# Kernel optimization log

Hardware: AMD Instinct MI355X
Metric: run time of the kernel (lower is better)

## Reference

```python
import jax, jax.numpy as jnp
import numpy as np

B, N = 2, 2000
C_IN, RH, RW = 256, 7, 7
D_FLAT = C_IN * RH * RW  # 12544
D_OUT = 1024
NUM_CLASSES = 10


def setup_inputs() -> dict:
    key = jax.random.key(0)
    ks = jax.random.split(key, 10)
    s1 = 1.0 / np.sqrt(D_FLAT)
    s2 = 1.0 / np.sqrt(D_OUT)
    return {
        "features": jax.random.normal(ks[0], (B, N, C_IN, RH, RW), jnp.float32),
        "boxes": jax.random.normal(ks[1], (B, N, 5), jnp.float32),
        "w1": jax.random.uniform(ks[2], (D_FLAT, D_OUT), jnp.float32, -s1, s1),
        "b1": jax.random.uniform(ks[3], (D_OUT,), jnp.float32, -s1, s1),
        "w2": jax.random.uniform(ks[4], (D_OUT, D_OUT), jnp.float32, -s2, s2),
        "b2": jax.random.uniform(ks[5], (D_OUT,), jnp.float32, -s2, s2),
        "wc": jax.random.uniform(ks[6], (D_OUT, NUM_CLASSES + 1), jnp.float32, -s2, s2),
        "bc": jax.random.uniform(ks[7], (NUM_CLASSES + 1,), jnp.float32, -s2, s2),
        "wr": jax.random.uniform(ks[8], (D_OUT, 5), jnp.float32, -s2, s2),
        "br": jax.random.uniform(ks[9], (5,), jnp.float32, -s2, s2),
    }


def reference(features, boxes, w1, b1, w2, b2, wc, bc, wr, br):
    # Flatten(start_dim=2): [B, N, C*7*7]
    x = features.reshape(B, N, D_FLAT)
    # fc: Linear -> ReLU -> Linear -> ReLU
    h = jax.nn.relu(jnp.einsum("bnd,de->bne", x, w1) + b1)
    h = jax.nn.relu(jnp.einsum("bnd,de->bne", h, w2) + b2)
    classification = jnp.einsum("bnd,dc->bnc", h, wc) + bc  # [B, N, num_classes+1]
    regression = jnp.einsum("bnd,dr->bnr", h, wr) + br      # [B, N, 5]
    boxes_out = boxes + regression
    rois = boxes
    return classification, boxes_out, rois
```

## Files before the change

### kernel.cpp

```cpp
#include <hip/hip_runtime.h>
#include <stdint.h>

#define GAS __attribute__((address_space(1)))
#define LAS __attribute__((address_space(3)))

typedef short bf16x8 __attribute__((ext_vector_type(8)));
typedef float f32x4 __attribute__((ext_vector_type(4)));
typedef unsigned short u16x8 __attribute__((ext_vector_type(8)));

__device__ __forceinline__ unsigned short f2bf(float f) {
  union { float f; uint32_t u; } v; v.f = f;
  uint32_t r = v.u + 0x7FFFu + ((v.u >> 16) & 1u);
  return (unsigned short)(r >> 16);
}

__global__ __launch_bounds__(256) void cvt_kernel(const float* __restrict__ src,
                                                  unsigned short* __restrict__ dst,
                                                  long n8) {
  long i = (long)blockIdx.x * blockDim.x + threadIdx.x;
  if (i >= n8) return;
  const float4* s4 = (const float4*)src;
  float4 a = s4[i * 2];
  float4 b = s4[i * 2 + 1];
  u16x8 o;
  o[0] = f2bf(a.x); o[1] = f2bf(a.y); o[2] = f2bf(a.z); o[3] = f2bf(a.w);
  o[4] = f2bf(b.x); o[5] = f2bf(b.y); o[6] = f2bf(b.z); o[7] = f2bf(b.w);
  ((u16x8*)dst)[i] = o;
}

__global__ __launch_bounds__(256) void transpose_cvt(const float* __restrict__ src,
                                                     unsigned short* __restrict__ dst,
                                                     int R, int C) {
  __shared__ unsigned short tile[32][33];
  int tx = threadIdx.x, ty = threadIdx.y;
  int r0 = blockIdx.y * 32, c0 = blockIdx.x * 32;
#pragma unroll
  for (int i = 0; i < 32; i += 8)
    tile[ty + i][tx] = f2bf(src[(long)(r0 + ty + i) * C + c0 + tx]);
  __syncthreads();
#pragma unroll
  for (int i = 0; i < 32; i += 8)
    dst[(long)(c0 + ty + i) * R + r0 + tx] = tile[tx][ty + i];
}

__global__ __launch_bounds__(256) void bias_relu_cvt(const float* __restrict__ acc,
                                                     const float* __restrict__ bias,
                                                     unsigned short* __restrict__ dst) {
  long i = (long)blockIdx.x * 256 + threadIdx.x;
  const float4* a4 = (const float4*)acc;
  float4 a = a4[i * 2];
  float4 b = a4[i * 2 + 1];
  int col = (int)((i * 8) & 1023);
  const float4* b4 = (const float4*)(bias + col);
  float4 ba = b4[0], bb = b4[1];
  u16x8 o;
  o[0] = f2bf(fmaxf(a.x + ba.x, 0.f)); o[1] = f2bf(fmaxf(a.y + ba.y, 0.f));
  o[2] = f2bf(fmaxf(a.z + ba.z, 0.f)); o[3] = f2bf(fmaxf(a.w + ba.w, 0.f));
  o[4] = f2bf(fmaxf(b.x + bb.x, 0.f)); o[5] = f2bf(fmaxf(b.y + bb.y, 0.f));
  o[6] = f2bf(fmaxf(b.z + bb.z, 0.f)); o[7] = f2bf(fmaxf(b.w + bb.w, 0.f));
  ((u16x8*)dst)[i] = o;
}

__global__ __launch_bounds__(256, 2) void gemm1_atomic(const unsigned short* __restrict__ A,
                                                       const unsigned short* __restrict__ Bt,
                                                       float* __restrict__ Cv, int M, int K,
                                                       int kIters) {
  __shared__ unsigned short lA[128 * 64];
  __shared__ unsigned short lB[128 * 64];
  const int tid = threadIdx.x;
  const int lane = tid & 63;
  const int wave = tid >> 6;
  const int wm = wave >> 1, wn = wave & 1;

  const int b = blockIdx.x;
  const int xcd = b & 7;
  const int slot = b >> 3;
  const int bx = slot & 7;
  const int pg = xcd * 16 + (slot >> 3);
  const int by = pg & 31;
  const int bz = pg >> 5;

  const long rowBase = (long)by * 128;
  const long colBase = (long)bx * 128;
  const int kStart = bz * kIters * 64;

  f32x4 acc[4][4];
#pragma unroll
  for (int i = 0; i < 4; i++)
#pragma unroll
    for (int j = 0; j < 4; j++) acc[i][j] = (f32x4){0.f, 0.f, 0.f, 0.f};

  long gA[4], gB[4];
#pragma unroll
  for (int it = 0; it < 4; ++it) {
    int f = it * 256 + tid;
    int r = f >> 3;
    int q = f & 7;
    int kq = ((q ^ (r & 7)) * 8) + kStart;
    long ar = rowBase + r;
    if (ar >= M) ar = M - 1;
    gA[it] = ar * (long)K + kq;
    gB[it] = ((long)(colBase + r)) * K + kq;
  }

  for (int ki = 0; ki < kIters; ++ki) {
    const long kc = (long)ki * 64;
#pragma unroll
    for (int it = 0; it < 4; ++it) {
      int f = it * 256 + tid;
      __builtin_amdgcn_global_load_lds((const GAS void*)(A + gA[it] + kc),
                                       (LAS void*)(lA + f * 8), 16, 0, 0);
    }
#pragma unroll
    for (int it = 0; it < 4; ++it) {
      int f = it * 256 + tid;
      __builtin_amdgcn_global_load_lds((const GAS void*)(Bt + gB[it] + kc),
                                       (LAS void*)(lB + f * 8), 16, 0, 0);
    }
    __syncthreads();
#pragma unroll
    for (int ks = 0; ks < 64; ks += 32) {
      bf16x8 af[4], bf[4];
      const int c = (ks >> 3) + (lane >> 4);
      const int slotk = (c ^ (lane & 7)) << 3;
      const int mr = wm * 64 + (lane & 15);
      const int nr = wn * 64 + (lane & 15);
#pragma unroll
      for (int i = 0; i < 4; i++)
        af[i] = *(const bf16x8*)(lA + (mr + i * 16) * 64 + slotk);
#pragma unroll
      for (int i = 0; i < 4; i++)
        bf[i] = *(const bf16x8*)(lB + (nr + i * 16) * 64 + slotk);
#pragma unroll
      for (int i = 0; i < 4; i++)
#pragma unroll
        for (int j = 0; j < 4; j++)
          acc[i][j] = __builtin_amdgcn_mfma_f32_16x16x32_bf16(af[i], bf[j], acc[i][j], 0, 0, 0);
    }
    __syncthreads();
  }

  const int cq = lane & 15;
  const int rq = (lane >> 4) * 4;
#pragma unroll
  for (int i = 0; i < 4; i++) {
#pragma unroll
    for (int j = 0; j < 4; j++) {
      int col = (int)colBase + wn * 64 + j * 16 + cq;
#pragma unroll
      for (int r = 0; r < 4; r++) {
        long grow = rowBase + wm * 64 + i * 16 + rq + r;
        if (grow < M) unsafeAtomicAdd(&Cv[grow * 1024 + col], acc[i][j][r]);
      }
    }
  }
}

__global__ __launch_bounds__(256, 2) void gemm2_direct(const unsigned short* __restrict__ A,
                                                       const unsigned short* __restrict__ Bt,
                                                       const float* __restrict__ bias,
                                                       float* __restrict__ Cv, int M) {
  const int K = 1024;
  __shared__ unsigned short lA[128 * 64];
  __shared__ unsigned short lB[64 * 64];
  const int tid = threadIdx.x;
  const int lane = tid & 63;
  const int wave = tid >> 6;
  const int wm = wave >> 1, wn = wave & 1;

  const int b = blockIdx.x;
  const int xcd = b & 7;
  const int slot = b >> 3;
  const int bx = slot & 15;
  const int by = xcd * 4 + (slot >> 4);

  const long rowBase = (long)by * 128;
  const long colBase = (long)bx * 64;

  f32x4 acc[4][2];
#pragma unroll
  for (int i = 0; i < 4; i++)
#pragma unroll
    for (int j = 0; j < 2; j++) acc[i][j] = (f32x4){0.f, 0.f, 0.f, 0.f};

  long gA[4], gB[2];
#pragma unroll
  for (int it = 0; it < 4; ++it) {
    int f = it * 256 + tid;
    int r = f >> 3;
    int q = f & 7;
    int kq = (q ^ (r & 7)) * 8;
    long ar = rowBase + r;
    if (ar >= M) ar = M - 1;
    gA[it] = ar * (long)K + kq;
  }
#pragma unroll
  for (int it = 0; it < 2; ++it) {
    int f = it * 256 + tid;
    int r = f >> 3;
    int q = f & 7;
    int kq = (q ^ (r & 7)) * 8;
    gB[it] = ((long)(colBase + r)) * K + kq;
  }

  for (int ki = 0; ki < 16; ++ki) {
    const long kc = (long)ki * 64;
#pragma unroll
    for (int it = 0; it < 4; ++it) {
      int f = it * 256 + tid;
      __builtin_amdgcn_global_load_lds((const GAS void*)(A + gA[it] + kc),
                                       (LAS void*)(lA + f * 8), 16, 0, 0);
    }
#pragma unroll
    for (int it = 0; it < 2; ++it) {
      int f = it * 256 + tid;
      __builtin_amdgcn_global_load_lds((const GAS void*)(Bt + gB[it] + kc),
                                       (LAS void*)(lB + f * 8), 16, 0, 0);
    }
    __syncthreads();
#pragma unroll
    for (int ks = 0; ks < 64; ks += 32) {
      bf16x8 af[4], bf[2];
      const int c = (ks >> 3) + (lane >> 4);
      const int slotk = (c ^ (lane & 7)) << 3;
      const int mr = wm * 64 + (lane & 15);
      const int nr = wn * 32 + (lane & 15);
#pragma unroll
      for (int i = 0; i < 4; i++)
        af[i] = *(const bf16x8*)(lA + (mr + i * 16) * 64 + slotk);
#pragma unroll
      for (int j = 0; j < 2; j++)
        bf[j] = *(const bf16x8*)(lB + (nr + j * 16) * 64 + slotk);
#pragma unroll
      for (int i = 0; i < 4; i++)
#pragma unroll
        for (int j = 0; j < 2; j++)
          acc[i][j] = __builtin_amdgcn_mfma_f32_16x16x32_bf16(af[i], bf[j], acc[i][j], 0, 0, 0);
    }
    __syncthreads();
  }

  const int cq = lane & 15;
  const int rq = (lane >> 4) * 4;
#pragma unroll
  for (int i = 0; i < 4; i++) {
#pragma unroll
    for (int j = 0; j < 2; j++) {
      int col = (int)colBase + wn * 32 + j * 16 + cq;
      float bv = bias[col];
#pragma unroll
      for (int r = 0; r < 4; r++) {
        long grow = rowBase + wm * 64 + i * 16 + rq + r;
        if (grow < M) {
          float v = acc[i][j][r] + bv;
          Cv[grow * 1024 + col] = v > 0.f ? v : 0.f;
        }
      }
    }
  }
}

__global__ __launch_bounds__(256) void head_kernel(
    const float* __restrict__ H2, const float* __restrict__ wc, const float* __restrict__ bc,
    const float* __restrict__ wr, const float* __restrict__ br, const float* __restrict__ boxes,
    float* __restrict__ cls, float* __restrict__ bout, float* __restrict__ rois) {
  const int lane = threadIdx.x & 63;
  const int wave = threadIdx.x >> 6;
  const int row = blockIdx.x * 4 + wave;
  const float* h = H2 + (long)row * 1024;
  float acc[16];
#pragma unroll
  for (int c = 0; c < 16; c++) acc[c] = 0.f;
#pragma unroll
  for (int i = 0; i < 16; i++) {
    int d = i * 64 + lane;
    float hv = h[d];
#pragma unroll
    for (int c = 0; c < 11; c++) acc[c] += hv * wc[d * 11 + c];
#pragma unroll
    for (int c = 0; c < 5; c++) acc[11 + c] += hv * wr[d * 5 + c];
  }
#pragma unroll
  for (int off = 32; off >= 1; off >>= 1) {
#pragma unroll
    for (int c = 0; c < 16; c++) acc[c] += __shfl_down(acc[c], off);
  }
  if (lane == 0) {
#pragma unroll
    for (int c = 0; c < 11; c++) cls[row * 11 + c] = acc[c] + bc[c];
#pragma unroll
    for (int c = 0; c < 5; c++) {
      float rg = acc[11 + c] + br[c];
      float bx = boxes[row * 5 + c];
      bout[row * 5 + c] = bx + rg;
      rois[row * 5 + c] = bx;
    }
  }
}

extern "C" void kernel_launch(void* const* d_in, const int* in_sizes, int n_in,
                              void* d_out, int out_size, void* d_ws, size_t ws_size,
                              hipStream_t stream) {
  const float* features = (const float*)d_in[0];
  const float* boxes = (const float*)d_in[1];
  const float* w1 = (const float*)d_in[2];
  const float* b1 = (const float*)d_in[3];
  const float* w2 = (const float*)d_in[4];
  const float* b2 = (const float*)d_in[5];
  const float* wc = (const float*)d_in[6];
  const float* bc = (const float*)d_in[7];
  const float* wr = (const float*)d_in[8];
  const float* br = (const float*)d_in[9];

  char* ws = (char*)d_ws;
  unsigned short* Xb  = (unsigned short*)ws;
  unsigned short* W1T = (unsigned short*)(ws + 100352000);
  unsigned short* W2T = (unsigned short*)(ws + 126042112);
  unsigned short* H1  = (unsigned short*)(ws + 128139264);
  float*          H1f = (float*)(ws + 136331264);
  float*          H2  = (float*)(ws + 152715264);

  hipMemsetAsync(H1f, 0, 16384000, stream);
  cvt_kernel<<<24500, 256, 0, stream>>>(features, Xb, 6272000);
  transpose_cvt<<<dim3(32, 392), dim3(32, 8), 0, stream>>>(w1, W1T, 12544, 1024);
  transpose_cvt<<<dim3(32, 32), dim3(32, 8), 0, stream>>>(w2, W2T, 1024, 1024);
  gemm1_atomic<<<1024, 256, 0, stream>>>(Xb, W1T, H1f, 4000, 12544, 49);
  bias_relu_cvt<<<2000, 256, 0, stream>>>(H1f, b1, H1);
  gemm2_direct<<<512, 256, 0, stream>>>(H1, W2T, b2, H2, 4000);
  float* cls = (float*)d_out;
  float* bout = cls + 44000;
  float* rois = cls + 64000;
  head_kernel<<<1000, 256, 0, stream>>>(H2, wc, bc, wr, br, boxes, cls, bout, rois);
}
```

Measured before the change: 529.8 us.

## Fuse feature fp32-to-bf16 conversion into GEMM1 with register prefetch

```diff
diff --git a/kernel.cpp b/kernel.cpp
--- a/kernel.cpp
+++ b/kernel.cpp
@@ -12,20 +12,6 @@
   union { float f; uint32_t u; } v; v.f = f;
   uint32_t r = v.u + 0x7FFFu + ((v.u >> 16) & 1u);
   return (unsigned short)(r >> 16);
-}
-
-__global__ __launch_bounds__(256) void cvt_kernel(const float* __restrict__ src,
-                                                  unsigned short* __restrict__ dst,
-                                                  long n8) {
-  long i = (long)blockIdx.x * blockDim.x + threadIdx.x;
-  if (i >= n8) return;
-  const float4* s4 = (const float4*)src;
-  float4 a = s4[i * 2];
-  float4 b = s4[i * 2 + 1];
-  u16x8 o;
-  o[0] = f2bf(a.x); o[1] = f2bf(a.y); o[2] = f2bf(a.z); o[3] = f2bf(a.w);
-  o[4] = f2bf(b.x); o[5] = f2bf(b.y); o[6] = f2bf(b.z); o[7] = f2bf(b.w);
-  ((u16x8*)dst)[i] = o;
 }
 
 __global__ __launch_bounds__(256) void transpose_cvt(const float* __restrict__ src,
@@ -61,10 +47,10 @@
   ((u16x8*)dst)[i] = o;
 }
 
-__global__ __launch_bounds__(256, 2) void gemm1_atomic(const unsigned short* __restrict__ A,
-                                                       const unsigned short* __restrict__ Bt,
-                                                       float* __restrict__ Cv, int M, int K,
-                                                       int kIters) {
+__global__ __launch_bounds__(256, 2) void gemm1_fused(const float* __restrict__ A,
+                                                      const unsigned short* __restrict__ Bt,
+                                                      float* __restrict__ Cv, int M, int K,
+                                                      int kIters) {
   __shared__ unsigned short lA[128 * 64];
   __shared__ unsigned short lB[128 * 64];
   const int tid = threadIdx.x;
@@ -90,7 +76,7 @@
 #pragma unroll
     for (int j = 0; j < 4; j++) acc[i][j] = (f32x4){0.f, 0.f, 0.f, 0.f};
 
-  long gA[4], gB[4];
+  int gAi[4], gBi[4];
 #pragma unroll
   for (int it = 0; it < 4; ++it) {
     int f = it * 256 + tid;
@@ -99,8 +85,17 @@
     int kq = ((q ^ (r & 7)) * 8) + kStart;
     long ar = rowBase + r;
     if (ar >= M) ar = M - 1;
-    gA[it] = ar * (long)K + kq;
-    gB[it] = ((long)(colBase + r)) * K + kq;
+    gAi[it] = (int)(ar * (long)K + kq);
+    gBi[it] = (int)((colBase + r) * (long)K + kq);
+  }
+
+  const uint4* A4 = (const uint4*)A;
+  uint4 pf[8];
+#pragma unroll
+  for (int it = 0; it < 4; ++it) {
+    long fi = ((long)gAi[it]) >> 2;
+    pf[2 * it] = A4[fi];
+    pf[2 * it + 1] = A4[fi + 1];
   }
 
   for (int ki = 0; ki < kIters; ++ki) {
@@ -108,19 +103,32 @@
 #pragma unroll
     for (int it = 0; it < 4; ++it) {
       int f = it * 256 + tid;
-      __builtin_amdgcn_global_load_lds((const GAS void*)(A + gA[it] + kc),
-                                       (LAS void*)(lA + f * 8), 16, 0, 0);
+      __builtin_amdgcn_global_load_lds((const GAS void*)(Bt + gBi[it] + kc),
+                                       (LAS void*)(lB + f * 8), 16, 0, 0);
     }
 #pragma unroll
     for (int it = 0; it < 4; ++it) {
       int f = it * 256 + tid;
-      __builtin_amdgcn_global_load_lds((const GAS void*)(Bt + gB[it] + kc),
-                                       (LAS void*)(lB + f * 8), 16, 0, 0);
+      uint4 lo = pf[2 * it], hi = pf[2 * it + 1];
+      uint4 o;
+      o.x = __builtin_amdgcn_perm(lo.y, lo.x, 0x07060302u);
+      o.y = __builtin_amdgcn_perm(lo.w, lo.z, 0x07060302u);
+      o.z = __builtin_amdgcn_perm(hi.y, hi.x, 0x07060302u);
+      o.w = __builtin_amdgcn_perm(hi.w, hi.z, 0x07060302u);
+      *(uint4*)(lA + f * 8) = o;
+    }
+    if (ki + 1 < kIters) {
+#pragma unroll
+      for (int it = 0; it < 4; ++it) {
+        long fi = ((long)gAi[it] + kc + 64) >> 2;
+        pf[2 * it] = A4[fi];
+        pf[2 * it + 1] = A4[fi + 1];
+      }
     }
     __syncthreads();
 #pragma unroll
     for (int ks = 0; ks < 64; ks += 32) {
-      bf16x8 af[4], bf[4];
+      bf16x8 af[4], bfr[4];
       const int c = (ks >> 3) + (lane >> 4);
       const int slotk = (c ^ (lane & 7)) << 3;
       const int mr = wm * 64 + (lane & 15);
@@ -130,12 +138,12 @@
         af[i] = *(const bf16x8*)(lA + (mr + i * 16) * 64 + slotk);
 #pragma unroll
       for (int i = 0; i < 4; i++)
-        bf[i] = *(const bf16x8*)(lB + (nr + i * 16) * 64 + slotk);
+        bfr[i] = *(const bf16x8*)(lB + (nr + i * 16) * 64 + slotk);
 #pragma unroll
       for (int i = 0; i < 4; i++)
 #pragma unroll
         for (int j = 0; j < 4; j++)
-          acc[i][j] = __builtin_amdgcn_mfma_f32_16x16x32_bf16(af[i], bf[j], acc[i][j], 0, 0, 0);
+          acc[i][j] = __builtin_amdgcn_mfma_f32_16x16x32_bf16(af[i], bfr[j], acc[i][j], 0, 0, 0);
     }
     __syncthreads();
   }
@@ -220,7 +228,7 @@
     __syncthreads();
 #pragma unroll
     for (int ks = 0; ks < 64; ks += 32) {
-      bf16x8 af[4], bf[2];
+      bf16x8 af[4], bfr[2];
       const int c = (ks >> 3) + (lane >> 4);
       const int slotk = (c ^ (lane & 7)) << 3;
       const int mr = wm * 64 + (lane & 15);
@@ -230,12 +238,12 @@
         af[i] = *(const bf16x8*)(lA + (mr + i * 16) * 64 + slotk);
 #pragma unroll
       for (int j = 0; j < 2; j++)
-        bf[j] = *(const bf16x8*)(lB + (nr + j * 16) * 64 + slotk);
+        bfr[j] = *(const bf16x8*)(lB + (nr + j * 16) * 64 + slotk);
 #pragma unroll
       for (int i = 0; i < 4; i++)
 #pragma unroll
         for (int j = 0; j < 2; j++)
-          acc[i][j] = __builtin_amdgcn_mfma_f32_16x16x32_bf16(af[i], bf[j], acc[i][j], 0, 0, 0);
+          acc[i][j] = __builtin_amdgcn_mfma_f32_16x16x32_bf16(af[i], bfr[j], acc[i][j], 0, 0, 0);
     }
     __syncthreads();
   }
@@ -313,18 +321,16 @@
   const float* br = (const float*)d_in[9];
 
   char* ws = (char*)d_ws;
-  unsigned short* Xb  = (unsigned short*)ws;
-  unsigned short* W1T = (unsigned short*)(ws + 100352000);
-  unsigned short* W2T = (unsigned short*)(ws + 126042112);
-  unsigned short* H1  = (unsigned short*)(ws + 128139264);
-  float*          H1f = (float*)(ws + 136331264);
-  float*          H2  = (float*)(ws + 152715264);
+  unsigned short* W1T = (unsigned short*)ws;
+  unsigned short* W2T = (unsigned short*)(ws + 25690112);
+  unsigned short* H1  = (unsigned short*)(ws + 27787264);
+  float*          H1f = (float*)(ws + 35979264);
+  float*          H2  = (float*)(ws + 52363264);
 
   hipMemsetAsync(H1f, 0, 16384000, stream);
-  cvt_kernel<<<24500, 256, 0, stream>>>(features, Xb, 6272000);
   transpose_cvt<<<dim3(32, 392), dim3(32, 8), 0, stream>>>(w1, W1T, 12544, 1024);
   transpose_cvt<<<dim3(32, 32), dim3(32, 8), 0, stream>>>(w2, W2T, 1024, 1024);
-  gemm1_atomic<<<1024, 256, 0, stream>>>(Xb, W1T, H1f, 4000, 12544, 49);
+  gemm1_fused<<<1024, 256, 0, stream>>>(features, W1T, H1f, 4000, 12544, 49);
   bias_relu_cvt<<<2000, 256, 0, stream>>>(H1f, b1, H1);
   gemm2_direct<<<512, 256, 0, stream>>>(H1, W2T, b2, H2, 4000);
   float* cls = (float*)d_out;
```

New measurement: 549.8 us. 3.8% more time.
